# Optimization experiments

Hardware: AMD Instinct MI355X
Metric: run time of the kernel (lower is better)

Reference implementation:

```python
import jax, jax.numpy as jnp
import numpy as np

EPS = 1e-06

def elu_feature_map(x):
    # elu(x) + 1, matching torch.nn.functional.elu default alpha=1
    return jax.nn.elu(x) + 1.0

def setup_inputs() -> dict:
    key = jax.random.key(0)
    k1, k2, k3 = jax.random.split(key, 3)
    n, L, h, e = 4, 8192, 8, 64
    queries = jax.random.normal(k1, (n, L, h, e), dtype=jnp.float32)
    keys = jax.random.normal(k2, (n, L, h, e), dtype=jnp.float32)
    values = jax.random.normal(k3, (n, L, h, e), dtype=jnp.float32)
    return {"queries": queries, "keys": keys, "values": values}

def reference(queries, keys, values):
    n, l, h, e = queries.shape
    softmax_temp = e ** (-0.25)
    q = elu_feature_map(queries * softmax_temp)   # [n, l, h, e]
    k = elu_feature_map(keys * softmax_temp)      # [n, s, h, e]
    # kv: sum over sequence of outer products k (x) v -> [n, h, d_v, e]
    kv = jnp.einsum('nshd,nshm->nhmd', k, values)
    # normalizer z = 1 / (q . sum_s k)
    z = 1.0 / (jnp.einsum('nlhd,nhd->nlh', q, k.sum(axis=1)) + EPS)
    v = jnp.einsum('nlhd,nhmd,nlh->nlhm', q, kv, z)
    return v
```

## Files before the change

### kernel.cpp

```cpp
#include <hip/hip_runtime.h>

#define N_      4
#define L_      8192
#define H_      8
#define E_      64
#define NH_     (N_ * H_)
#define STRIDE_ (H_ * E_)
#define SPLIT_  32
#define RPB_    (L_ / SPLIT_)
#define NCH_    (RPB_ / 16)

#define PKV_FLOATS ((size_t)NH_ * SPLIT_ * E_ * E_)
#define PKS_FLOATS ((size_t)NH_ * SPLIT_ * E_)
#define KVT_FLOATS ((size_t)NH_ * E_ * E_ / 2)
#define PKS_OFF  PKV_FLOATS
#define KVT_OFF  (PKV_FLOATS + PKS_FLOATS)
#define KSUM_OFF (KVT_OFF + KVT_FLOATS)

typedef short bf16x8 __attribute__((ext_vector_type(8)));
typedef float f32x16 __attribute__((ext_vector_type(16)));

__device__ __forceinline__ float featmap(float x) {
    float xs = x * 0.35355339059327373f;
    return xs > 0.0f ? xs + 1.0f : __expf(xs);
}
__device__ __forceinline__ unsigned short f2bf(float f) {
    union { float f; unsigned u; } c{f};
    unsigned r = c.u + 0x7FFFu + ((c.u >> 16) & 1u);
    return (unsigned short)(r >> 16);
}

__global__ __launch_bounds__(256) void la_kv(
    const float* __restrict__ keys, const float* __restrict__ values,
    float* __restrict__ pkv, float* __restrict__ pks)
{
    const int blk = blockIdx.x;
    const int nh = blk / SPLIT_, chunk = blk % SPLIT_;
    const int n = nh / H_, h = nh % H_;
    const int t = threadIdx.x, l = t & 63;
    const int w = t >> 6, wd = w >> 1, wm = w & 1;
    const int lm = l & 31, lh = l >> 5;

    const size_t base = (size_t)n * (L_ * H_ * E_) + (size_t)h * E_;
    const int s0 = chunk * RPB_;
    const float* kcol = keys   + base + (size_t)s0 * STRIDE_ + 32 * wd + lm;
    const float* vcol = values + base + (size_t)s0 * STRIDE_ + 32 * wm + lm;

    f32x16 acc = {0,0,0,0,0,0,0,0,0,0,0,0,0,0,0,0};
    float ksum = 0.f;

    float ka[2][8], va[2][8];
    #pragma unroll
    for (int j = 0; j < 8; ++j) {
        ka[0][j] = kcol[(size_t)(8 * lh + j) * STRIDE_];
        va[0][j] = vcol[(size_t)(8 * lh + j) * STRIDE_];
    }

    #pragma unroll
    for (int c = 0; c < NCH_; ++c) {
        const int cur = c & 1, nxt = cur ^ 1;
        if (c + 1 < NCH_) {
            #pragma unroll
            for (int j = 0; j < 8; ++j) {
                ka[nxt][j] = kcol[(size_t)((c + 1) * 16 + 8 * lh + j) * STRIDE_];
                va[nxt][j] = vcol[(size_t)((c + 1) * 16 + 8 * lh + j) * STRIDE_];
            }
        }
        bf16x8 af, bf;
        #pragma unroll
        for (int j = 0; j < 8; ++j) {
            const float kf = featmap(ka[cur][j]);
            ksum += kf;
            af[j] = (short)f2bf(kf);
            bf[j] = (short)f2bf(va[cur][j]);
        }
        acc = __builtin_amdgcn_mfma_f32_32x32x16_bf16(af, bf, acc, 0, 0, 0);
    }

    float* dst = pkv + (size_t)blk * (E_ * E_);
    #pragma unroll
    for (int r = 0; r < 16; ++r) {
        const int ro = (r & 3) + 8 * (r >> 2) + 4 * lh;
        dst[(32 * wd + ro) * E_ + 32 * wm + lm] = acc[r];
    }

    ksum += __shfl_xor(ksum, 32);
    if (wm == 0 && lh == 0)
        pks[(size_t)blk * E_ + 32 * wd + lm] = ksum;
}

__global__ __launch_bounds__(256) void la_reduce(
    const float* __restrict__ pkv, const float* __restrict__ pks,
    unsigned short* __restrict__ kvt, float* __restrict__ ksum)
{
    const int b = blockIdx.x, nh = b >> 4, sl = b & 15;
    const int e = sl * 256 + threadIdx.x;
    const float* src = pkv + (size_t)nh * SPLIT_ * (E_ * E_) + e;
    float s = 0.f;
    #pragma unroll
    for (int c = 0; c < SPLIT_; ++c) s += src[(size_t)c * (E_ * E_)];
    const int d = e >> 6, m = e & 63;
    kvt[(size_t)nh * (E_ * E_) + m * E_ + d] = f2bf(s);

    if (sl == 0 && threadIdx.x < E_) {
        const float* sp = pks + (size_t)nh * SPLIT_ * E_ + threadIdx.x;
        float ss = 0.f;
        #pragma unroll
        for (int c = 0; c < SPLIT_; ++c) ss += sp[c * E_];
        ksum[nh * E_ + threadIdx.x] = ss;
    }
}

__global__ __launch_bounds__(256) void la_out(
    const float* __restrict__ q, const unsigned short* __restrict__ kvt,
    const float* __restrict__ ksum, float* __restrict__ out)
{
    const int blk = blockIdx.x, nh = blk >> 5, tile = blk & 31;
    const int n = nh / H_, h = nh % H_;
    const int t = threadIdx.x, l = t & 63, w = t >> 6;
    const int lm = l & 31, lh = l >> 5;

    __shared__ float zbuf[4][32];

    const unsigned short* kb = kvt + (size_t)nh * (E_ * E_);
    const float* ks = ksum + nh * E_;

    bf16x8 bfr[4][2];
    float4 kr[4][2];
    #pragma unroll
    for (int st = 0; st < 4; ++st) {
        #pragma unroll
        for (int c = 0; c < 2; ++c)
            bfr[st][c] = *(const bf16x8*)&kb[(32 * c + lm) * E_ + st * 16 + 8 * lh];
        kr[st][0] = *(const float4*)&ks[st * 16 + 8 * lh];
        kr[st][1] = *(const float4*)&ks[st * 16 + 8 * lh + 4];
    }

    const size_t base = (size_t)n * (L_ * H_ * E_) + (size_t)h * E_;

    #pragma unroll
    for (int bnd = 0; bnd < 2; ++bnd) {
        const int l0 = tile * 256 + w * 64 + bnd * 32;
        const float* qp = q + base + (size_t)(l0 + lm) * STRIDE_ + 8 * lh;

        float4 qa[4], qb[4];
        #pragma unroll
        for (int st = 0; st < 4; ++st) {
            qa[st] = *(const float4*)(qp + st * 16);
            qb[st] = *(const float4*)(qp + st * 16 + 4);
        }

        float zd = 0.f;
        bf16x8 af[4];
        #pragma unroll
        for (int st = 0; st < 4; ++st) {
            const float f0 = featmap(qa[st].x), f1 = featmap(qa[st].y),
                        f2 = featmap(qa[st].z), f3 = featmap(qa[st].w);
            const float g0 = featmap(qb[st].x), g1 = featmap(qb[st].y),
                        g2 = featmap(qb[st].z), g3 = featmap(qb[st].w);
            zd += f0 * kr[st][0].x + f1 * kr[st][0].y + f2 * kr[st][0].z + f3 * kr[st][0].w
                + g0 * kr[st][1].x + g1 * kr[st][1].y + g2 * kr[st][1].z + g3 * kr[st][1].w;
            bf16x8 a;
            a[0] = (short)f2bf(f0); a[1] = (short)f2bf(f1);
            a[2] = (short)f2bf(f2); a[3] = (short)f2bf(f3);
            a[4] = (short)f2bf(g0); a[5] = (short)f2bf(g1);
            a[6] = (short)f2bf(g2); a[7] = (short)f2bf(g3);
            af[st] = a;
        }
        zd += __shfl_xor(zd, 32);
        const float z = 1.0f / (zd + 1e-6f);
        if (l < 32) zbuf[w][l] = z;
        __builtin_amdgcn_wave_barrier();

        f32x16 c0 = {0,0,0,0,0,0,0,0,0,0,0,0,0,0,0,0};
        f32x16 c1 = {0,0,0,0,0,0,0,0,0,0,0,0,0,0,0,0};
        #pragma unroll
        for (int st = 0; st < 4; ++st) {
            c0 = __builtin_amdgcn_mfma_f32_32x32x16_bf16(af[st], bfr[st][0], c0, 0, 0, 0);
            c1 = __builtin_amdgcn_mfma_f32_32x32x16_bf16(af[st], bfr[st][1], c1, 0, 0, 0);
        }

        float* op = out + base + (size_t)l0 * STRIDE_ + lm;
        #pragma unroll
        for (int r = 0; r < 16; ++r) {
            const int ro = (r & 3) + 8 * (r >> 2) + 4 * lh;
            const float zz = zbuf[w][ro];
            op[(size_t)ro * STRIDE_]      = c0[r] * zz;
            op[(size_t)ro * STRIDE_ + 32] = c1[r] * zz;
        }
        __builtin_amdgcn_wave_barrier();
    }
}

extern "C" void kernel_launch(void* const* d_in, const int* in_sizes, int n_in,
                              void* d_out, int out_size, void* d_ws, size_t ws_size,
                              hipStream_t stream) {
    (void)in_sizes; (void)n_in; (void)out_size; (void)ws_size;
    const float* qq = (const float*)d_in[0];
    const float* kk = (const float*)d_in[1];
    const float* vv = (const float*)d_in[2];
    float* outp = (float*)d_out;
    float* ws   = (float*)d_ws;

    float* pkv = ws;
    float* pks = ws + PKS_OFF;
    unsigned short* kvt = (unsigned short*)(ws + KVT_OFF);
    float* ksm = ws + KSUM_OFF;

    la_kv<<<NH_ * SPLIT_, 256, 0, stream>>>(kk, vv, pkv, pks);
    la_reduce<<<NH_ * 16, 256, 0, stream>>>(pkv, pks, kvt, ksm);
    la_out<<<NH_ * 32, 256, 0, stream>>>(qq, kvt, ksm, outp);
}
```

Measured before the change: 68.31 us.

## Split KV chunk across two wave groups and use packed bf16 conversion

```diff
diff --git a/kernel.cpp b/kernel.cpp
--- a/kernel.cpp
+++ b/kernel.cpp
@@ -8,7 +8,8 @@
 #define STRIDE_ (H_ * E_)
 #define SPLIT_  32
 #define RPB_    (L_ / SPLIT_)
-#define NCH_    (RPB_ / 16)
+#define RPW_    (RPB_ / 2)
+#define NCH_    (RPW_ / 16)
 
 #define PKV_FLOATS ((size_t)NH_ * SPLIT_ * E_ * E_)
 #define PKS_FLOATS ((size_t)NH_ * SPLIT_ * E_)
@@ -19,6 +20,7 @@
 
 typedef short bf16x8 __attribute__((ext_vector_type(8)));
 typedef float f32x16 __attribute__((ext_vector_type(16)));
+union bfpack { bf16x8 v; unsigned u[4]; };
 
 __device__ __forceinline__ float featmap(float x) {
     float xs = x * 0.35355339059327373f;
@@ -29,8 +31,13 @@
     unsigned r = c.u + 0x7FFFu + ((c.u >> 16) & 1u);
     return (unsigned short)(r >> 16);
 }
-
-__global__ __launch_bounds__(256) void la_kv(
+__device__ __forceinline__ unsigned cvt_pk_bf16(float lo, float hi) {
+    unsigned r;
+    asm("v_cvt_pk_bf16_f32 %0, %1, %2" : "=v"(r) : "v"(lo), "v"(hi));
+    return r;
+}
+
+__global__ __launch_bounds__(512, 8) void la_kv(
     const float* __restrict__ keys, const float* __restrict__ values,
     float* __restrict__ pkv, float* __restrict__ pks)
 {
@@ -38,11 +45,15 @@
     const int nh = blk / SPLIT_, chunk = blk % SPLIT_;
     const int n = nh / H_, h = nh % H_;
     const int t = threadIdx.x, l = t & 63;
-    const int w = t >> 6, wd = w >> 1, wm = w & 1;
+    const int w = t >> 6;
+    const int sh = w >> 2, wd = (w >> 1) & 1, wm = w & 1;
     const int lm = l & 31, lh = l >> 5;
 
+    __shared__ float red[4][32 * 32];
+    __shared__ float ksl[2][2][32];
+
     const size_t base = (size_t)n * (L_ * H_ * E_) + (size_t)h * E_;
-    const int s0 = chunk * RPB_;
+    const int s0 = chunk * RPB_ + sh * RPW_;
     const float* kcol = keys   + base + (size_t)s0 * STRIDE_ + 32 * wd + lm;
     const float* vcol = values + base + (size_t)s0 * STRIDE_ + 32 * wm + lm;
 
@@ -66,27 +77,44 @@
                 va[nxt][j] = vcol[(size_t)((c + 1) * 16 + 8 * lh + j) * STRIDE_];
             }
         }
-        bf16x8 af, bf;
+        float kf[8];
         #pragma unroll
         for (int j = 0; j < 8; ++j) {
-            const float kf = featmap(ka[cur][j]);
-            ksum += kf;
-            af[j] = (short)f2bf(kf);
-            bf[j] = (short)f2bf(va[cur][j]);
-        }
-        acc = __builtin_amdgcn_mfma_f32_32x32x16_bf16(af, bf, acc, 0, 0, 0);
-    }
-
-    float* dst = pkv + (size_t)blk * (E_ * E_);
-    #pragma unroll
-    for (int r = 0; r < 16; ++r) {
-        const int ro = (r & 3) + 8 * (r >> 2) + 4 * lh;
-        dst[(32 * wd + ro) * E_ + 32 * wm + lm] = acc[r];
+            kf[j] = featmap(ka[cur][j]);
+            ksum += kf[j];
+        }
+        bfpack af, bf;
+        #pragma unroll
+        for (int p = 0; p < 4; ++p) {
+            af.u[p] = cvt_pk_bf16(kf[2 * p], kf[2 * p + 1]);
+            bf.u[p] = cvt_pk_bf16(va[cur][2 * p], va[cur][2 * p + 1]);
+        }
+        acc = __builtin_amdgcn_mfma_f32_32x32x16_bf16(af.v, bf.v, acc, 0, 0, 0);
     }
 
     ksum += __shfl_xor(ksum, 32);
-    if (wm == 0 && lh == 0)
-        pks[(size_t)blk * E_ + 32 * wd + lm] = ksum;
+    if (wm == 0 && lh == 0) ksl[sh][wd][lm] = ksum;
+
+    const int tile = wd * 2 + wm;
+    if (sh == 1) {
+        #pragma unroll
+        for (int r = 0; r < 16; ++r) {
+            const int ro = (r & 3) + 8 * (r >> 2) + 4 * lh;
+            red[tile][ro * 32 + lm] = acc[r];
+        }
+    }
+    __syncthreads();
+    if (sh == 0) {
+        float* dst = pkv + (size_t)blk * (E_ * E_);
+        #pragma unroll
+        for (int r = 0; r < 16; ++r) {
+            const int ro = (r & 3) + 8 * (r >> 2) + 4 * lh;
+            dst[(32 * wd + ro) * E_ + 32 * wm + lm] =
+                acc[r] + red[tile][ro * 32 + lm];
+        }
+    }
+    if (t < E_)
+        pks[(size_t)blk * E_ + t] = ksl[0][t >> 5][t & 31] + ksl[1][t >> 5][t & 31];
 }
 
 __global__ __launch_bounds__(256) void la_reduce(
@@ -160,12 +188,12 @@
                         g2 = featmap(qb[st].z), g3 = featmap(qb[st].w);
             zd += f0 * kr[st][0].x + f1 * kr[st][0].y + f2 * kr[st][0].z + f3 * kr[st][0].w
                 + g0 * kr[st][1].x + g1 * kr[st][1].y + g2 * kr[st][1].z + g3 * kr[st][1].w;
-            bf16x8 a;
-            a[0] = (short)f2bf(f0); a[1] = (short)f2bf(f1);
-            a[2] = (short)f2bf(f2); a[3] = (short)f2bf(f3);
-            a[4] = (short)f2bf(g0); a[5] = (short)f2bf(g1);
-            a[6] = (short)f2bf(g2); a[7] = (short)f2bf(g3);
-            af[st] = a;
+            bfpack a;
+            a.u[0] = cvt_pk_bf16(f0, f1);
+            a.u[1] = cvt_pk_bf16(f2, f3);
+            a.u[2] = cvt_pk_bf16(g0, g1);
+            a.u[3] = cvt_pk_bf16(g2, g3);
+            af[st] = a.v;
         }
         zd += __shfl_xor(zd, 32);
         const float z = 1.0f / (zd + 1e-6f);
@@ -207,7 +235,7 @@
     unsigned short* kvt = (unsigned short*)(ws + KVT_OFF);
     float* ksm = ws + KSUM_OFF;
 
-    la_kv<<<NH_ * SPLIT_, 256, 0, stream>>>(kk, vv, pkv, pks);
+    la_kv<<<NH_ * SPLIT_, 512, 0, stream>>>(kk, vv, pkv, pks);
     la_reduce<<<NH_ * 16, 256, 0, stream>>>(pkv, pks, kvt, ksm);
     la_out<<<NH_ * 32, 256, 0, stream>>>(qq, kvt, ksm, outp);
 }
```

Measured after the change: 118.7 us. +73.8%, slower.

## Stage K/V through swizzled LDS with vectorized loads and packed bf16 converts

Applied to the files above, without the earlier changes.

```diff
diff --git a/kernel.cpp b/kernel.cpp
--- a/kernel.cpp
+++ b/kernel.cpp
@@ -8,14 +8,8 @@
 #define STRIDE_ (H_ * E_)
 #define SPLIT_  32
 #define RPB_    (L_ / SPLIT_)
-#define NCH_    (RPB_ / 16)
-
-#define PKV_FLOATS ((size_t)NH_ * SPLIT_ * E_ * E_)
-#define PKS_FLOATS ((size_t)NH_ * SPLIT_ * E_)
-#define KVT_FLOATS ((size_t)NH_ * E_ * E_ / 2)
-#define PKS_OFF  PKV_FLOATS
-#define KVT_OFF  (PKV_FLOATS + PKS_FLOATS)
-#define KSUM_OFF (KVT_OFF + KVT_FLOATS)
+#define CHR_    64
+#define NCHK_   (RPB_ / CHR_)
 
 typedef short bf16x8 __attribute__((ext_vector_type(8)));
 typedef float f32x16 __attribute__((ext_vector_type(16)));
@@ -28,6 +22,14 @@
     union { float f; unsigned u; } c{f};
     unsigned r = c.u + 0x7FFFu + ((c.u >> 16) & 1u);
     return (unsigned short)(r >> 16);
+}
+__device__ __forceinline__ unsigned cvt_pk_bf16(float lo, float hi) {
+    unsigned r;
+    asm("v_cvt_pk_bf16_f32 %0, %1, %2" : "=v"(r) : "v"(lo), "v"(hi));
+    return r;
+}
+__device__ __forceinline__ int swz_slot(int d, int sp4) {
+    return (sp4 ^ (d & 7) ^ ((d >> 2) & 7)) & 7;
 }
 
 __global__ __launch_bounds__(256) void la_kv(
@@ -40,41 +42,75 @@
     const int t = threadIdx.x, l = t & 63;
     const int w = t >> 6, wd = w >> 1, wm = w & 1;
     const int lm = l & 31, lh = l >> 5;
+    const int pr = t >> 3, c = t & 7;
+
+    __shared__ unsigned Kb[2][CHR_][32];
+    __shared__ unsigned Vb[2][CHR_][32];
+
+    f32x16 acc = {0,0,0,0,0,0,0,0,0,0,0,0,0,0,0,0};
+    float ksp[8] = {0.f,0.f,0.f,0.f,0.f,0.f,0.f,0.f};
 
     const size_t base = (size_t)n * (L_ * H_ * E_) + (size_t)h * E_;
-    const int s0 = chunk * RPB_;
-    const float* kcol = keys   + base + (size_t)s0 * STRIDE_ + 32 * wd + lm;
-    const float* vcol = values + base + (size_t)s0 * STRIDE_ + 32 * wm + lm;
-
-    f32x16 acc = {0,0,0,0,0,0,0,0,0,0,0,0,0,0,0,0};
-    float ksum = 0.f;
-
-    float ka[2][8], va[2][8];
-    #pragma unroll
-    for (int j = 0; j < 8; ++j) {
-        ka[0][j] = kcol[(size_t)(8 * lh + j) * STRIDE_];
-        va[0][j] = vcol[(size_t)(8 * lh + j) * STRIDE_];
-    }
-
-    #pragma unroll
-    for (int c = 0; c < NCH_; ++c) {
-        const int cur = c & 1, nxt = cur ^ 1;
-        if (c + 1 < NCH_) {
-            #pragma unroll
-            for (int j = 0; j < 8; ++j) {
-                ka[nxt][j] = kcol[(size_t)((c + 1) * 16 + 8 * lh + j) * STRIDE_];
-                va[nxt][j] = vcol[(size_t)((c + 1) * 16 + 8 * lh + j) * STRIDE_];
-            }
-        }
-        bf16x8 af, bf;
-        #pragma unroll
-        for (int j = 0; j < 8; ++j) {
-            const float kf = featmap(ka[cur][j]);
-            ksum += kf;
-            af[j] = (short)f2bf(kf);
-            bf[j] = (short)f2bf(va[cur][j]);
-        }
-        acc = __builtin_amdgcn_mfma_f32_32x32x16_bf16(af, bf, acc, 0, 0, 0);
+    const size_t rbase = base + (size_t)(chunk * RPB_ + 2 * pr) * STRIDE_ + 4 * c;
+
+    float4 kr0 = *(const float4*)(keys + rbase);
+    float4 kr1 = *(const float4*)(keys + rbase + 32);
+    float4 kr2 = *(const float4*)(keys + rbase + STRIDE_);
+    float4 kr3 = *(const float4*)(keys + rbase + STRIDE_ + 32);
+    float4 vr0 = *(const float4*)(values + rbase);
+    float4 vr1 = *(const float4*)(values + rbase + 32);
+    float4 vr2 = *(const float4*)(values + rbase + STRIDE_);
+    float4 vr3 = *(const float4*)(values + rbase + STRIDE_ + 32);
+
+    #pragma unroll
+    for (int ch = 0; ch < NCHK_; ++ch) {
+        const int buf = ch & 1;
+        float a0[4] = {kr0.x, kr0.y, kr0.z, kr0.w};
+        float a1[4] = {kr1.x, kr1.y, kr1.z, kr1.w};
+        float a2[4] = {kr2.x, kr2.y, kr2.z, kr2.w};
+        float a3[4] = {kr3.x, kr3.y, kr3.z, kr3.w};
+        float b0[4] = {vr0.x, vr0.y, vr0.z, vr0.w};
+        float b1[4] = {vr1.x, vr1.y, vr1.z, vr1.w};
+        float b2[4] = {vr2.x, vr2.y, vr2.z, vr2.w};
+        float b3[4] = {vr3.x, vr3.y, vr3.z, vr3.w};
+
+        #pragma unroll
+        for (int i = 0; i < 4; ++i) {
+            const float f0 = featmap(a0[i]), f1 = featmap(a1[i]);
+            const float f2 = featmap(a2[i]), f3 = featmap(a3[i]);
+            ksp[i]     += f0 + f2;
+            ksp[4 + i] += f1 + f3;
+            const int dl = 4 * c + i, dh = 32 + 4 * c + i;
+            const int wl = swz_slot(dl, pr >> 2) * 4 + (pr & 3);
+            const int wh = swz_slot(dh, pr >> 2) * 4 + (pr & 3);
+            Kb[buf][dl][wl] = cvt_pk_bf16(f0, f2);
+            Kb[buf][dh][wh] = cvt_pk_bf16(f1, f3);
+            Vb[buf][dl][wl] = cvt_pk_bf16(b0[i], b2[i]);
+            Vb[buf][dh][wh] = cvt_pk_bf16(b1[i], b3[i]);
+        }
+
+        if (ch + 1 < NCHK_) {
+            const size_t nb = rbase + (size_t)(ch + 1) * CHR_ * STRIDE_;
+            kr0 = *(const float4*)(keys + nb);
+            kr1 = *(const float4*)(keys + nb + 32);
+            kr2 = *(const float4*)(keys + nb + STRIDE_);
+            kr3 = *(const float4*)(keys + nb + STRIDE_ + 32);
+            vr0 = *(const float4*)(values + nb);
+            vr1 = *(const float4*)(values + nb + 32);
+            vr2 = *(const float4*)(values + nb + STRIDE_);
+            vr3 = *(const float4*)(values + nb + STRIDE_ + 32);
+        }
+
+        __syncthreads();
+
+        const int rk = 32 * wd + lm, rv = 32 * wm + lm;
+        #pragma unroll
+        for (int m = 0; m < 4; ++m) {
+            const int sa = ((2 * m + lh) ^ (lm & 7) ^ (lm >> 2)) & 7;
+            bf16x8 af = *(const bf16x8*)&Kb[buf][rk][sa * 4];
+            bf16x8 bv = *(const bf16x8*)&Vb[buf][rv][sa * 4];
+            acc = __builtin_amdgcn_mfma_f32_32x32x16_bf16(af, bv, acc, 0, 0, 0);
+        }
     }
 
     float* dst = pkv + (size_t)blk * (E_ * E_);
@@ -84,9 +120,18 @@
         dst[(32 * wd + ro) * E_ + 32 * wm + lm] = acc[r];
     }
 
-    ksum += __shfl_xor(ksum, 32);
-    if (wm == 0 && lh == 0)
-        pks[(size_t)blk * E_ + 32 * wd + lm] = ksum;
+    __syncthreads();
+    float* ksb = (float*)&Kb[0][0][0];
+    *(float4*)&ksb[t * 8]     = make_float4(ksp[0], ksp[1], ksp[2], ksp[3]);
+    *(float4*)&ksb[t * 8 + 4] = make_float4(ksp[4], ksp[5], ksp[6], ksp[7]);
+    __syncthreads();
+    if (t < E_) {
+        const int cc = (t & 31) >> 2, e = (t >> 5) * 4 + (t & 3);
+        float s = 0.f;
+        #pragma unroll
+        for (int pp = 0; pp < 32; ++pp) s += ksb[(pp * 8 + cc) * 8 + e];
+        pks[(size_t)blk * E_ + t] = s;
+    }
 }
 
 __global__ __launch_bounds__(256) void la_reduce(
@@ -160,12 +205,12 @@
                         g2 = featmap(qb[st].z), g3 = featmap(qb[st].w);
             zd += f0 * kr[st][0].x + f1 * kr[st][0].y + f2 * kr[st][0].z + f3 * kr[st][0].w
                 + g0 * kr[st][1].x + g1 * kr[st][1].y + g2 * kr[st][1].z + g3 * kr[st][1].w;
-            bf16x8 a;
-            a[0] = (short)f2bf(f0); a[1] = (short)f2bf(f1);
-            a[2] = (short)f2bf(f2); a[3] = (short)f2bf(f3);
-            a[4] = (short)f2bf(g0); a[5] = (short)f2bf(g1);
-            a[6] = (short)f2bf(g2); a[7] = (short)f2bf(g3);
-            af[st] = a;
+            union { bf16x8 v; unsigned u[4]; } a;
+            a.u[0] = cvt_pk_bf16(f0, f1);
+            a.u[1] = cvt_pk_bf16(f2, f3);
+            a.u[2] = cvt_pk_bf16(g0, g1);
+            a.u[3] = cvt_pk_bf16(g2, g3);
+            af[st] = a.v;
         }
         zd += __shfl_xor(zd, 32);
         const float z = 1.0f / (zd + 1e-6f);
@@ -203,9 +248,9 @@
     float* ws   = (float*)d_ws;
 
     float* pkv = ws;
-    float* pks = ws + PKS_OFF;
-    unsigned short* kvt = (unsigned short*)(ws + KVT_OFF);
-    float* ksm = ws + KSUM_OFF;
+    float* pks = ws + (size_t)NH_ * SPLIT_ * (E_ * E_);
+    unsigned short* kvt = (unsigned short*)(pks + (size_t)NH_ * SPLIT_ * E_);
+    float* ksm = (float*)(kvt + (size_t)NH_ * (E_ * E_));
 
     la_kv<<<NH_ * SPLIT_, 256, 0, stream>>>(kk, vv, pkv, pks);
     la_reduce<<<NH_ * 16, 256, 0, stream>>>(pkv, pks, kvt, ksm);
```

New measurement: 65.78 us. -3.7%, faster.

## Restage KV kernel through swizzled LDS with coalesced float4 row loads for all heads

Applied to the files above, without the earlier changes.

```diff
diff --git a/kernel.cpp b/kernel.cpp
--- a/kernel.cpp
+++ b/kernel.cpp
@@ -5,17 +5,16 @@
 #define H_      8
 #define E_      64
 #define NH_     (N_ * H_)
-#define STRIDE_ (H_ * E_)
-#define SPLIT_  32
-#define RPB_    (L_ / SPLIT_)
-#define NCH_    (RPB_ / 16)
-
-#define PKV_FLOATS ((size_t)NH_ * SPLIT_ * E_ * E_)
-#define PKS_FLOATS ((size_t)NH_ * SPLIT_ * E_)
-#define KVT_FLOATS ((size_t)NH_ * E_ * E_ / 2)
-#define PKS_OFF  PKV_FLOATS
-#define KVT_OFF  (PKV_FLOATS + PKS_FLOATS)
-#define KSUM_OFF (KVT_OFF + KVT_FLOATS)
+#define ROWF_   512
+#define CKB_    64
+#define RPB_    128
+
+#define PKV_F  ((size_t)N_ * CKB_ * H_ * E_ * E_)
+#define PKS_F  ((size_t)N_ * CKB_ * H_ * E_)
+#define KVT_F  ((size_t)NH_ * E_ * E_ / 2)
+#define PKS_OFF  PKV_F
+#define KVT_OFF  (PKV_F + PKS_F)
+#define KSUM_OFF (KVT_OFF + KVT_F)
 
 typedef short bf16x8 __attribute__((ext_vector_type(8)));
 typedef float f32x16 __attribute__((ext_vector_type(16)));
@@ -29,64 +28,115 @@
     unsigned r = c.u + 0x7FFFu + ((c.u >> 16) & 1u);
     return (unsigned short)(r >> 16);
 }
-
-__global__ __launch_bounds__(256) void la_kv(
+__device__ __forceinline__ unsigned cvt_pk_bf16(float lo, float hi) {
+    unsigned r;
+    asm("v_cvt_pk_bf16_f32 %0, %1, %2" : "=v"(r) : "v"(lo), "v"(hi));
+    return r;
+}
+
+__global__ __launch_bounds__(512) void la_kv(
     const float* __restrict__ keys, const float* __restrict__ values,
     float* __restrict__ pkv, float* __restrict__ pks)
 {
     const int blk = blockIdx.x;
-    const int nh = blk / SPLIT_, chunk = blk % SPLIT_;
-    const int n = nh / H_, h = nh % H_;
-    const int t = threadIdx.x, l = t & 63;
-    const int w = t >> 6, wd = w >> 1, wm = w & 1;
+    const int n = blk / CKB_, cki = blk % CKB_;
+    const int t = threadIdx.x, l = t & 63, w = t >> 6;
     const int lm = l & 31, lh = l >> 5;
-
-    const size_t base = (size_t)n * (L_ * H_ * E_) + (size_t)h * E_;
-    const int s0 = chunk * RPB_;
-    const float* kcol = keys   + base + (size_t)s0 * STRIDE_ + 32 * wd + lm;
-    const float* vcol = values + base + (size_t)s0 * STRIDE_ + 32 * wm + lm;
-
-    f32x16 acc = {0,0,0,0,0,0,0,0,0,0,0,0,0,0,0,0};
-    float ksum = 0.f;
-
-    float ka[2][8], va[2][8];
-    #pragma unroll
-    for (int j = 0; j < 8; ++j) {
-        ka[0][j] = kcol[(size_t)(8 * lh + j) * STRIDE_];
-        va[0][j] = vcol[(size_t)(8 * lh + j) * STRIDE_];
-    }
-
-    #pragma unroll
-    for (int c = 0; c < NCH_; ++c) {
-        const int cur = c & 1, nxt = cur ^ 1;
-        if (c + 1 < NCH_) {
-            #pragma unroll
-            for (int j = 0; j < 8; ++j) {
-                ka[nxt][j] = kcol[(size_t)((c + 1) * 16 + 8 * lh + j) * STRIDE_];
-                va[nxt][j] = vcol[(size_t)((c + 1) * 16 + 8 * lh + j) * STRIDE_];
-            }
-        }
-        bf16x8 af, bf;
-        #pragma unroll
-        for (int j = 0; j < 8; ++j) {
-            const float kf = featmap(ka[cur][j]);
-            ksum += kf;
-            af[j] = (short)f2bf(kf);
-            bf[j] = (short)f2bf(va[cur][j]);
-        }
-        acc = __builtin_amdgcn_mfma_f32_32x32x16_bf16(af, bf, acc, 0, 0, 0);
-    }
-
-    float* dst = pkv + (size_t)blk * (E_ * E_);
-    #pragma unroll
-    for (int r = 0; r < 16; ++r) {
-        const int ro = (r & 3) + 8 * (r >> 2) + 4 * lh;
-        dst[(32 * wd + ro) * E_ + 32 * wm + lm] = acc[r];
-    }
-
-    ksum += __shfl_xor(ksum, 32);
-    if (wm == 0 && lh == 0)
-        pks[(size_t)blk * E_ + 32 * wd + lm] = ksum;
+    const int spo = t & 3;
+    const int c4  = t >> 2;
+    const int sh  = c4 >> 4;
+    const int sd0 = 4 * (c4 & 15);
+
+    __shared__ unsigned Kb[H_][E_][32];
+    __shared__ unsigned Vb[H_][E_][32];
+
+    f32x16 acc[4];
+    #pragma unroll
+    for (int q = 0; q < 4; ++q)
+        acc[q] = (f32x16){0,0,0,0,0,0,0,0,0,0,0,0,0,0,0,0};
+    float ksp[4] = {0.f, 0.f, 0.f, 0.f};
+
+    const size_t rowbase = ((size_t)n * L_ + (size_t)cki * RPB_) * ROWF_ + 4 * c4;
+    float4 kld[2][2], vld[2][2];
+
+#define LOADSR(CH, SR, B) {                                                   \
+    const size_t o_ = rowbase + (size_t)((CH) * 64 + (SR) * 8 + 2 * spo) * ROWF_; \
+    kld[B][0] = *(const float4*)(keys + o_);                                  \
+    kld[B][1] = *(const float4*)(keys + o_ + ROWF_);                          \
+    vld[B][0] = *(const float4*)(values + o_);                                \
+    vld[B][1] = *(const float4*)(values + o_ + ROWF_); }
+
+#define STORESR(SR, B) {                                                      \
+    const float fe_[4] = {featmap(kld[B][0].x), featmap(kld[B][0].y),         \
+                          featmap(kld[B][0].z), featmap(kld[B][0].w)};        \
+    const float fo_[4] = {featmap(kld[B][1].x), featmap(kld[B][1].y),         \
+                          featmap(kld[B][1].z), featmap(kld[B][1].w)};        \
+    const float ve_[4] = {vld[B][0].x, vld[B][0].y, vld[B][0].z, vld[B][0].w};\
+    const float vo_[4] = {vld[B][1].x, vld[B][1].y, vld[B][1].z, vld[B][1].w};\
+    _Pragma("unroll")                                                         \
+    for (int j_ = 0; j_ < 4; ++j_) {                                          \
+        ksp[j_] += fe_[j_] + fo_[j_];                                         \
+        const int d_ = sd0 + j_;                                              \
+        const int sl_ = ((SR) ^ (d_ & 7) ^ ((d_ >> 2) & 7)) & 7;              \
+        Kb[sh][d_][sl_ * 4 + spo] = cvt_pk_bf16(fe_[j_], fo_[j_]);            \
+        Vb[sh][d_][sl_ * 4 + spo] = cvt_pk_bf16(ve_[j_], vo_[j_]); } }
+
+#define COMPUTECH() {                                                         \
+    _Pragma("unroll")                                                         \
+    for (int m_ = 0; m_ < 4; ++m_) {                                          \
+        const int sa_ = ((2 * m_ + lh) ^ (lm & 7) ^ (lm >> 2)) & 7;           \
+        bf16x8 a0_ = *(const bf16x8*)&Kb[w][lm][sa_ * 4];                     \
+        bf16x8 a1_ = *(const bf16x8*)&Kb[w][32 + lm][sa_ * 4];                \
+        bf16x8 b0_ = *(const bf16x8*)&Vb[w][lm][sa_ * 4];                     \
+        bf16x8 b1_ = *(const bf16x8*)&Vb[w][32 + lm][sa_ * 4];                \
+        acc[0] = __builtin_amdgcn_mfma_f32_32x32x16_bf16(a0_, b0_, acc[0], 0, 0, 0); \
+        acc[1] = __builtin_amdgcn_mfma_f32_32x32x16_bf16(a0_, b1_, acc[1], 0, 0, 0); \
+        acc[2] = __builtin_amdgcn_mfma_f32_32x32x16_bf16(a1_, b0_, acc[2], 0, 0, 0); \
+        acc[3] = __builtin_amdgcn_mfma_f32_32x32x16_bf16(a1_, b1_, acc[3], 0, 0, 0); } }
+
+    LOADSR(0, 0, 0);
+    #pragma unroll
+    for (int sr = 0; sr < 8; ++sr) {
+        if (sr < 7) { LOADSR(0, sr + 1, (sr + 1) & 1); }
+        else        { LOADSR(1, 0, 0); }
+        STORESR(sr, sr & 1);
+    }
+    __syncthreads();
+    COMPUTECH();
+    __syncthreads();
+    #pragma unroll
+    for (int sr = 0; sr < 8; ++sr) {
+        if (sr < 7) { LOADSR(1, sr + 1, (sr + 1) & 1); }
+        STORESR(sr, sr & 1);
+    }
+    __syncthreads();
+    COMPUTECH();
+#undef LOADSR
+#undef STORESR
+#undef COMPUTECH
+
+    float* dst = pkv + ((size_t)blk * H_ + w) * (E_ * E_);
+    #pragma unroll
+    for (int q = 0; q < 4; ++q) {
+        const int wd = q >> 1, wm = q & 1;
+        #pragma unroll
+        for (int r = 0; r < 16; ++r) {
+            const int ro = (r & 3) + 8 * (r >> 2) + 4 * lh;
+            dst[(32 * wd + ro) * E_ + 32 * wm + lm] = acc[q][r];
+        }
+    }
+
+    __syncthreads();
+    float* ksb = (float*)&Kb[0][0][0];
+    *(float4*)&ksb[t * 4] = make_float4(ksp[0], ksp[1], ksp[2], ksp[3]);
+    __syncthreads();
+    {
+        const int hq = t >> 6, dq = t & 63;
+        const int c4r = (hq << 4) | (dq >> 2), jr = dq & 3;
+        float s = ksb[(c4r * 4 + 0) * 4 + jr] + ksb[(c4r * 4 + 1) * 4 + jr]
+                + ksb[(c4r * 4 + 2) * 4 + jr] + ksb[(c4r * 4 + 3) * 4 + jr];
+        pks[(size_t)blk * 512 + t] = s;
+    }
 }
 
 __global__ __launch_bounds__(256) void la_reduce(
@@ -94,19 +144,20 @@
     unsigned short* __restrict__ kvt, float* __restrict__ ksum)
 {
     const int b = blockIdx.x, nh = b >> 4, sl = b & 15;
+    const int n2 = nh >> 3, h = nh & 7;
     const int e = sl * 256 + threadIdx.x;
-    const float* src = pkv + (size_t)nh * SPLIT_ * (E_ * E_) + e;
+    const float* src = pkv + ((size_t)(n2 * CKB_) * H_ + h) * (E_ * E_) + e;
     float s = 0.f;
     #pragma unroll
-    for (int c = 0; c < SPLIT_; ++c) s += src[(size_t)c * (E_ * E_)];
+    for (int c2 = 0; c2 < CKB_; ++c2) s += src[(size_t)c2 * H_ * (E_ * E_)];
     const int d = e >> 6, m = e & 63;
     kvt[(size_t)nh * (E_ * E_) + m * E_ + d] = f2bf(s);
 
     if (sl == 0 && threadIdx.x < E_) {
-        const float* sp = pks + (size_t)nh * SPLIT_ * E_ + threadIdx.x;
+        const float* sp = pks + (size_t)(n2 * CKB_) * 512 + h * E_ + threadIdx.x;
         float ss = 0.f;
         #pragma unroll
-        for (int c = 0; c < SPLIT_; ++c) ss += sp[c * E_];
+        for (int c2 = 0; c2 < CKB_; ++c2) ss += sp[(size_t)c2 * 512];
         ksum[nh * E_ + threadIdx.x] = ss;
     }
 }
@@ -141,7 +192,7 @@
     #pragma unroll
     for (int bnd = 0; bnd < 2; ++bnd) {
         const int l0 = tile * 256 + w * 64 + bnd * 32;
-        const float* qp = q + base + (size_t)(l0 + lm) * STRIDE_ + 8 * lh;
+        const float* qp = q + base + (size_t)(l0 + lm) * (H_ * E_) + 8 * lh;
 
         float4 qa[4], qb[4];
         #pragma unroll
@@ -160,12 +211,12 @@
                         g2 = featmap(qb[st].z), g3 = featmap(qb[st].w);
             zd += f0 * kr[st][0].x + f1 * kr[st][0].y + f2 * kr[st][0].z + f3 * kr[st][0].w
                 + g0 * kr[st][1].x + g1 * kr[st][1].y + g2 * kr[st][1].z + g3 * kr[st][1].w;
-            bf16x8 a;
-            a[0] = (short)f2bf(f0); a[1] = (short)f2bf(f1);
-            a[2] = (short)f2bf(f2); a[3] = (short)f2bf(f3);
-            a[4] = (short)f2bf(g0); a[5] = (short)f2bf(g1);
-            a[6] = (short)f2bf(g2); a[7] = (short)f2bf(g3);
-            af[st] = a;
+            union { bf16x8 v; unsigned u[4]; } a;
+            a.u[0] = cvt_pk_bf16(f0, f1);
+            a.u[1] = cvt_pk_bf16(f2, f3);
+            a.u[2] = cvt_pk_bf16(g0, g1);
+            a.u[3] = cvt_pk_bf16(g2, g3);
+            af[st] = a.v;
         }
         zd += __shfl_xor(zd, 32);
         const float z = 1.0f / (zd + 1e-6f);
@@ -180,13 +231,13 @@
             c1 = __builtin_amdgcn_mfma_f32_32x32x16_bf16(af[st], bfr[st][1], c1, 0, 0, 0);
         }
 
-        float* op = out + base + (size_t)l0 * STRIDE_ + lm;
+        float* op = out + base + (size_t)l0 * (H_ * E_) + lm;
         #pragma unroll
         for (int r = 0; r < 16; ++r) {
             const int ro = (r & 3) + 8 * (r >> 2) + 4 * lh;
             const float zz = zbuf[w][ro];
-            op[(size_t)ro * STRIDE_]      = c0[r] * zz;
-            op[(size_t)ro * STRIDE_ + 32] = c1[r] * zz;
+            op[(size_t)ro * (H_ * E_)]      = c0[r] * zz;
+            op[(size_t)ro * (H_ * E_) + 32] = c1[r] * zz;
         }
         __builtin_amdgcn_wave_barrier();
     }
@@ -207,7 +258,7 @@
     unsigned short* kvt = (unsigned short*)(ws + KVT_OFF);
     float* ksm = ws + KSUM_OFF;
 
-    la_kv<<<NH_ * SPLIT_, 256, 0, stream>>>(kk, vv, pkv, pks);
+    la_kv<<<N_ * CKB_, 512, 0, stream>>>(kk, vv, pkv, pks);
     la_reduce<<<NH_ * 16, 256, 0, stream>>>(pkv, pks, kvt, ksm);
     la_out<<<NH_ * 32, 256, 0, stream>>>(qq, kvt, ksm, outp);
 }
```

Result: slower. 85.88 us (+25.7%).
